# Kernel tuning notes

Measured on AMD Instinct MI355X. Metric: run time of the kernel, lower is better.

Reference implementation:

```python
import jax, jax.numpy as jnp
import numpy as np
from math import sqrt

D_MODEL = 1024
NUM_HEADS = 16
MASK_VAL = -100000000.0


def setup_inputs() -> dict:
    key = jax.random.key(0)
    k1, k2, k3, k4, k5 = jax.random.split(key, 5)
    scale = 1.0 / sqrt(D_MODEL)
    return {
        "in_features": jax.random.normal(k1, (2, 2048, D_MODEL), dtype=jnp.float32),
        "q_proj_weight": jax.random.normal(k2, (D_MODEL, D_MODEL), dtype=jnp.float32) * scale,
        "k_proj_weight": jax.random.normal(k3, (D_MODEL, D_MODEL), dtype=jnp.float32) * scale,
        "v_proj_weight": jax.random.normal(k4, (D_MODEL, D_MODEL), dtype=jnp.float32) * scale,
        "o_proj_weight": jax.random.normal(k5, (D_MODEL, D_MODEL), dtype=jnp.float32) * scale,
    }


def _proj_heads(x, w, h):
    # x: [b, s, d_in], w: [h*d, d_in] -> [b, h, s, d]
    d = w.shape[0] // h
    w = w.reshape(h, d, w.shape[1])
    return jnp.einsum('bsi,hdi->bhsd', x, w)


def reference(in_features, q_proj_weight, k_proj_weight, v_proj_weight, o_proj_weight):
    h = NUM_HEADS
    b, s, _ = in_features.shape
    q = _proj_heads(in_features, q_proj_weight, h)  # [b,h,s,dk]
    k = _proj_heads(in_features, k_proj_weight, h)
    v = _proj_heads(in_features, v_proj_weight, h)
    d_k = q.shape[-1]
    # additive causal mask: -1e8 above diagonal
    mask = jnp.triu(jnp.full((s, s), MASK_VAL, dtype=q.dtype), k=1)[None, None]
    scores = jnp.einsum('bhqd,bhkd->bhqk', q, k) / sqrt(d_k) + mask
    attn = jax.nn.softmax(scores, axis=-1)
    out = jnp.einsum('bhqk,bhkd->bhqd', attn, v)          # [b,h,s,dv]
    out = out.transpose(0, 2, 1, 3).reshape(b, s, -1)      # [b,s,h*dv]
    return jnp.einsum('bsv,mv->bsm', out, o_proj_weight)
```

## Files before the change

kernel.cpp:

```cpp
#include <hip/hip_runtime.h>
#include <hip/hip_bf16.h>
#include <stdint.h>
#include <type_traits>

typedef __bf16 bf16;
typedef __bf16 bf16x4 __attribute__((ext_vector_type(4)));
typedef __bf16 bf16x8 __attribute__((ext_vector_type(8)));
typedef float floatx4 __attribute__((ext_vector_type(4)));
typedef unsigned int u32;
typedef u32 u32x4 __attribute__((ext_vector_type(4)));

#define D_MODEL 1024
#define SEQ 2048
#define NHEADS 16
#define DH 64
#define BATCH 2
#define MROWS (BATCH * SEQ)

#define XELEMS ((size_t)MROWS * D_MODEL)
#define WELEMS ((size_t)D_MODEL * D_MODEL)
#define CVT_ELEMS (XELEMS + 4 * WELEMS)

__device__ __forceinline__ void gload_lds16(const void* g, void* l) {
  __builtin_amdgcn_global_load_lds(
      (const __attribute__((address_space(1))) u32*)g,
      (__attribute__((address_space(3))) u32*)l, 16, 0, 0);
}

__global__ __launch_bounds__(256) void cvt_f32_bf16(
    const float* __restrict__ s0, const float* __restrict__ s1,
    const float* __restrict__ s2, const float* __restrict__ s3,
    const float* __restrict__ s4, bf16* __restrict__ dst) {
  const size_t i = ((size_t)blockIdx.x * 256 + threadIdx.x) * 8;
  const float* src;
  size_t off;
  if (i < XELEMS) {
    src = s0; off = i;
  } else {
    const size_t j = i - XELEMS;
    const int r = (int)(j / WELEMS);
    src = (r == 0) ? s1 : (r == 1) ? s2 : (r == 2) ? s3 : s4;
    off = j - (size_t)r * WELEMS;
  }
  floatx4 f0 = *(const floatx4*)&src[off];
  floatx4 f1 = *(const floatx4*)&src[off + 4];
  bf16x8 o;
#pragma unroll
  for (int j = 0; j < 4; j++) { o[j] = (bf16)f0[j]; o[4 + j] = (bf16)f1[j]; }
  *(bf16x8*)&dst[i] = o;
}

#define QKV_ASLOT (256 * 64)
#define QKV_SLOT  (256 * 64 + 128 * 64)

__global__ __launch_bounds__(512) void gemm_qkv(
    const bf16* __restrict__ A, const bf16* __restrict__ W,
    bf16* __restrict__ Qo, bf16* __restrict__ Ko, bf16* __restrict__ Vto) {
  __shared__ bf16 sm[3 * QKV_SLOT];

  const int tid = threadIdx.x;
  const int lane = tid & 63;
  const int w = tid >> 6;
  const int lo16 = lane & 15;
  const int quad = lane >> 4;
  const int wy = w >> 1;
  const int wx = w & 1;

  const int n0 = blockIdx.x * 128;
  const int m0 = blockIdx.y * 256;

  const int sl = lane >> 3;
  const int sc = ((lane & 7) ^ sl) * 8;

  const floatx4 fz = {0.f, 0.f, 0.f, 0.f};
  floatx4 acc[4][4];
#pragma unroll
  for (int i = 0; i < 4; i++)
#pragma unroll
    for (int j = 0; j < 4; j++) acc[i][j] = fz;

  auto stage = [&](int t, int s) {
    bf16* As = &sm[s * QKV_SLOT];
    bf16* Bs = As + QKV_ASLOT;
    const int k0 = t * 64;
#pragma unroll
    for (int i = 0; i < 4; i++) {
      const int seg = w * 4 + i;
      const int row = seg * 8 + sl;
      gload_lds16(&A[(size_t)(m0 + row) * 1024 + k0 + sc], &As[seg * 512]);
    }
#pragma unroll
    for (int i = 0; i < 2; i++) {
      const int seg = w * 2 + i;
      const int row = seg * 8 + sl;
      gload_lds16(&W[(size_t)(n0 + row) * 1024 + k0 + sc], &Bs[seg * 512]);
    }
  };

  auto compute = [&](int s, auto vt) {
    constexpr bool VT = decltype(vt)::value;
    const bf16* As = &sm[s * QKV_SLOT];
    const bf16* Bs = As + QKV_ASLOT;
#pragma unroll
    for (int kk = 0; kk < 64; kk += 32) {
      bf16x8 af[4], bfr[4];
      const int cc = (kk >> 3) + quad;
#pragma unroll
      for (int t = 0; t < 4; t++) {
        const int ra = wy * 64 + t * 16 + lo16;
        const int rb = wx * 64 + t * 16 + lo16;
        af[t]  = *(const bf16x8*)&As[ra * 64 + ((cc ^ (ra & 7)) << 3)];
        bfr[t] = *(const bf16x8*)&Bs[rb * 64 + ((cc ^ (rb & 7)) << 3)];
      }
#pragma unroll
      for (int mt = 0; mt < 4; mt++)
#pragma unroll
        for (int nt = 0; nt < 4; nt++) {
          if constexpr (VT)
            acc[mt][nt] = __builtin_amdgcn_mfma_f32_16x16x32_bf16(bfr[nt], af[mt], acc[mt][nt], 0, 0, 0);
          else
            acc[mt][nt] = __builtin_amdgcn_mfma_f32_16x16x32_bf16(af[mt], bfr[nt], acc[mt][nt], 0, 0, 0);
        }
    }
  };

  auto step = [&](int t, int s, auto vt) {
    if (t + 2 < 16) stage(t + 2, (t + 2) % 3);
    compute(s, vt);
    if (t < 15) {
      if (t + 2 < 16) { asm volatile("s_waitcnt vmcnt(6)" ::: "memory"); }
      else            { asm volatile("s_waitcnt vmcnt(0)" ::: "memory"); }
      __builtin_amdgcn_s_barrier();
    }
  };

  auto mainloop = [&](auto vt) {
    stage(0, 0);
    stage(1, 1);
    asm volatile("s_waitcnt vmcnt(6)" ::: "memory");
    __builtin_amdgcn_s_barrier();
    for (int tb = 0; tb < 15; tb += 3) {
      step(tb + 0, 0, vt);
      step(tb + 1, 1, vt);
      step(tb + 2, 2, vt);
    }
    step(15, 0, vt);
  };
  if (n0 >= 2048) mainloop(std::true_type{}); else mainloop(std::false_type{});

  if (n0 < 2048) {
    bf16* C = (n0 < 1024) ? Qo : Ko;
    const int nc = (n0 < 1024) ? n0 : n0 - 1024;
#pragma unroll
    for (int mt = 0; mt < 4; mt++)
#pragma unroll
      for (int nt = 0; nt < 4; nt++)
#pragma unroll
        for (int r = 0; r < 4; r++) {
          const int row = m0 + wy * 64 + mt * 16 + quad * 4 + r;
          const int col = nc + wx * 64 + nt * 16 + lo16;
          C[(size_t)row * D_MODEL + col] = (bf16)acc[mt][nt][r];
        }
  } else {
    const int nv = n0 - 2048;
#pragma unroll
    for (int mt = 0; mt < 4; mt++)
#pragma unroll
      for (int nt = 0; nt < 4; nt++)
#pragma unroll
        for (int r = 0; r < 4; r++) {
          const int feat = nv + wx * 64 + nt * 16 + quad * 4 + r;
          const int tok  = m0 + wy * 64 + mt * 16 + lo16;
          const int hh = feat >> 6, dd = feat & 63;
          const int bb = tok >> 11, ss = tok & 2047;
          Vto[(size_t)((bb * NHEADS + hh) * DH + dd) * SEQ + ss] = (bf16)acc[mt][nt][r];
        }
  }
}

__global__ __launch_bounds__(256) void gemm_o(
    const bf16* __restrict__ A, const bf16* __restrict__ W,
    float* __restrict__ C) {
  __shared__ bf16 As[2 * 64 * 64];
  __shared__ bf16 Bs[2 * 128 * 64];

  const int tid = threadIdx.x;
  const int lane = tid & 63;
  const int w = tid >> 6;
  const int lo16 = lane & 15;
  const int quad = lane >> 4;
  const int wy = w >> 1, wx = w & 1;

  const int m0 = blockIdx.y * 64;
  const int n0 = blockIdx.x * 128;

  const int sl = lane >> 3;
  const int sc = ((lane & 7) ^ sl) * 8;

  const floatx4 fz = {0.f, 0.f, 0.f, 0.f};
  floatx4 acc[2][4];
#pragma unroll
  for (int i = 0; i < 2; i++)
#pragma unroll
    for (int j = 0; j < 4; j++) acc[i][j] = fz;

  for (int k0 = 0; k0 < 1024; k0 += 128) {
    __syncthreads();
#pragma unroll
    for (int kh = 0; kh < 2; kh++) {
#pragma unroll
      for (int i = 0; i < 2; i++) {
        const int seg = i * 4 + w;
        const int row = seg * 8 + sl;
        gload_lds16(&A[(size_t)(m0 + row) * 1024 + k0 + kh * 64 + sc],
                    &As[kh * 4096 + seg * 512]);
      }
#pragma unroll
      for (int i = 0; i < 4; i++) {
        const int seg = i * 4 + w;
        const int row = seg * 8 + sl;
        gload_lds16(&W[(size_t)(n0 + row) * 1024 + k0 + kh * 64 + sc],
                    &Bs[kh * 8192 + seg * 512]);
      }
    }
    __syncthreads();

#pragma unroll
    for (int kk = 0; kk < 128; kk += 32) {
      const int kh = kk >> 6;
      const int cc = ((kk & 63) >> 3) + quad;
      bf16x8 af[2], bfr[4];
#pragma unroll
      for (int t = 0; t < 2; t++) {
        const int ra = wy * 32 + t * 16 + lo16;
        af[t] = *(const bf16x8*)&As[kh * 4096 + ra * 64 + ((cc ^ (ra & 7)) << 3)];
      }
#pragma unroll
      for (int t = 0; t < 4; t++) {
        const int rb = wx * 64 + t * 16 + lo16;
        bfr[t] = *(const bf16x8*)&Bs[kh * 8192 + rb * 64 + ((cc ^ (rb & 7)) << 3)];
      }
#pragma unroll
      for (int mt = 0; mt < 2; mt++)
#pragma unroll
        for (int nt = 0; nt < 4; nt++)
          acc[mt][nt] = __builtin_amdgcn_mfma_f32_16x16x32_bf16(af[mt], bfr[nt], acc[mt][nt], 0, 0, 0);
    }
  }

#pragma unroll
  for (int mt = 0; mt < 2; mt++)
#pragma unroll
    for (int nt = 0; nt < 4; nt++)
#pragma unroll
      for (int r = 0; r < 4; r++) {
        const int row = m0 + wy * 32 + mt * 16 + quad * 4 + r;
        const int col = n0 + wx * 64 + nt * 16 + lo16;
        C[(size_t)row * D_MODEL + col] = acc[mt][nt][r];
      }
}

#define LPK 72
#define LPV 136

__global__ __launch_bounds__(512) void attn_causal(
    const bf16* __restrict__ Q, const bf16* __restrict__ Kg,
    const bf16* __restrict__ Vt, bf16* __restrict__ O) {
  __shared__ __align__(16) char smem[41984];
  bf16* Ks  = (bf16*)smem;
  bf16* VTs = (bf16*)(smem + 18432);
  float* Es = (float*)smem;

  const int tid = threadIdx.x;
  const int lane = tid & 63;
  const int wid = tid >> 6;
  const int g = wid >> 2;
  const int w4 = wid & 3;
  const int lo16 = lane & 15;
  const int quad = lane >> 4;

  const int x = blockIdx.x;
  const int qtA = x;
  const int qtB = 31 - x;
  const int nA = (qtA + 2) >> 1;
  const int nB = (qtB + 2) >> 1;
  const int h = blockIdx.y;
  const int b = blockIdx.z;
  const size_t base  = (size_t)b * SEQ * D_MODEL + (size_t)h * DH;
  const size_t baset = (size_t)(b * NHEADS + h) * DH * SEQ;

  const int rA = qtA * 64 + w4 * 16 + lo16;
  const int rB = qtB * 64 + w4 * 16 + lo16;
  bf16x8 qfA[2], qfB[2];
#pragma unroll
  for (int ks = 0; ks < 2; ks++) {
    qfA[ks] = *(const bf16x8*)&Q[base + (size_t)rA * D_MODEL + ks * 32 + quad * 8];
    qfB[ks] = *(const bf16x8*)&Q[base + (size_t)rB * D_MODEL + ks * 32 + quad * 8];
  }

  bf16x8 onesf;
#pragma unroll
  for (int j = 0; j < 8; j++) onesf[j] = (bf16)1.0f;

  const floatx4 fz = {0.f, 0.f, 0.f, 0.f};
  floatx4 oA[4], oB[4];
  floatx4 lA = fz, lB = fz;
#pragma unroll
  for (int i = 0; i < 4; i++) { oA[i] = fz; oB[i] = fz; }

  const int kr = tid >> 3;
  const int kc = (tid & 7) * 8;

  bf16x8 kvp[2], vvp[2];
#pragma unroll
  for (int c2 = 0; c2 < 2; c2++) {
    kvp[c2] = *(const bf16x8*)&Kg[base + (size_t)(c2 * 64 + kr) * D_MODEL + kc];
    vvp[c2] = *(const bf16x8*)&Vt[baset + (size_t)kr * SEQ + c2 * 64 + kc];
  }

  for (int c = 0; c < nB; c++) {
    const int j0 = c * 128;
    __syncthreads();
#pragma unroll
    for (int c2 = 0; c2 < 2; c2++) {
      *(bf16x8*)&Ks[(c2 * 64 + kr) * LPK + kc] = kvp[c2];
      *(bf16x8*)&VTs[kr * LPV + c2 * 64 + kc] = vvp[c2];
    }
    __syncthreads();

    if (c + 1 < nB) {
      const int j1 = j0 + 128;
#pragma unroll
      for (int c2 = 0; c2 < 2; c2++) {
        kvp[c2] = *(const bf16x8*)&Kg[base + (size_t)(j1 + c2 * 64 + kr) * D_MODEL + kc];
        vvp[c2] = *(const bf16x8*)&Vt[baset + (size_t)kr * SEQ + j1 + c2 * 64 + kc];
      }
    }

    auto compute = [&](int q0s, const bf16x8* qf, floatx4* oacc, floatx4& lacc,
                       bool diag) {
      floatx4 sacc[4];
#pragma unroll
      for (int n4 = 0; n4 < 4; n4++) sacc[n4] = fz;
#pragma unroll
      for (int n4 = 0; n4 < 4; n4++) {
        const int rk = g * 64 + n4 * 16 + lo16;
#pragma unroll
        for (int ks = 0; ks < 2; ks++) {
          bf16x8 kf = *(const bf16x8*)&Ks[rk * LPK + ks * 32 + quad * 8];
          sacc[n4] = __builtin_amdgcn_mfma_f32_16x16x32_bf16(kf, qf[ks], sacc[n4], 0, 0, 0);
        }
      }

      u32 wv[4][2];
      if (diag) {
        const int myq = q0s + w4 * 16 + lo16;
#pragma unroll
        for (int n4 = 0; n4 < 4; n4++) {
          float e[4];
#pragma unroll
          for (int r = 0; r < 4; r++) {
            const int kvb = j0 + g * 64 + n4 * 16 + quad * 4 + r;
            const float ev = __builtin_amdgcn_exp2f(fmaf(sacc[n4][r], 0.18033688f, -17.3123405f));
            e[r] = (kvb > myq) ? 0.f : ev;
          }
          asm("v_cvt_pk_bf16_f32 %0, %1, %2" : "=v"(wv[n4][0]) : "v"(e[0]), "v"(e[1]));
          asm("v_cvt_pk_bf16_f32 %0, %1, %2" : "=v"(wv[n4][1]) : "v"(e[2]), "v"(e[3]));
        }
      } else {
#pragma unroll
        for (int n4 = 0; n4 < 4; n4++) {
          float e[4];
#pragma unroll
          for (int r = 0; r < 4; r++)
            e[r] = __builtin_amdgcn_exp2f(fmaf(sacc[n4][r], 0.18033688f, -17.3123405f));
          asm("v_cvt_pk_bf16_f32 %0, %1, %2" : "=v"(wv[n4][0]) : "v"(e[0]), "v"(e[1]));
          asm("v_cvt_pk_bf16_f32 %0, %1, %2" : "=v"(wv[n4][1]) : "v"(e[2]), "v"(e[3]));
        }
      }

#pragma unroll
      for (int ks = 0; ks < 2; ks++) {
        u32 a0 = wv[2 * ks][0], b0 = wv[2 * ks + 1][0];
        u32 a1 = wv[2 * ks][1], b1 = wv[2 * ks + 1][1];
        asm("v_permlane32_swap_b32 %0, %1" : "+v"(a0), "+v"(b0));
        asm("v_permlane16_swap_b32 %0, %1" : "+v"(a0), "+v"(b0));
        asm("v_permlane32_swap_b32 %0, %1" : "+v"(a1), "+v"(b1));
        asm("v_permlane16_swap_b32 %0, %1" : "+v"(a1), "+v"(b1));
        u32x4 fw = {a0, a1, b0, b1};
        const bf16x8 pf = __builtin_bit_cast(bf16x8, fw);
#pragma unroll
        for (int dt = 0; dt < 4; dt++) {
          bf16x8 vf = *(const bf16x8*)&VTs[(dt * 16 + lo16) * LPV + g * 64 + ks * 32 + quad * 8];
          oacc[dt] = __builtin_amdgcn_mfma_f32_16x16x32_bf16(pf, vf, oacc[dt], 0, 0, 0);
        }
        lacc = __builtin_amdgcn_mfma_f32_16x16x32_bf16(pf, onesf, lacc, 0, 0, 0);
      }
    };

    compute(qtB * 64, qfB, oB, lB, c == nB - 1);
    if (c < nA) compute(qtA * 64, qfA, oA, lA, c == nA - 1);
  }

  __syncthreads();
  if (g == 1) {
    float* e = &Es[(w4 * 64 + lane) * 41];
#pragma unroll
    for (int dt = 0; dt < 4; dt++)
#pragma unroll
      for (int r = 0; r < 4; r++) e[dt * 4 + r] = oA[dt][r];
#pragma unroll
    for (int r = 0; r < 4; r++) e[16 + r] = lA[r];
#pragma unroll
    for (int dt = 0; dt < 4; dt++)
#pragma unroll
      for (int r = 0; r < 4; r++) e[20 + dt * 4 + r] = oB[dt][r];
#pragma unroll
    for (int r = 0; r < 4; r++) e[36 + r] = lB[r];
  }
  __syncthreads();
  if (g == 0) {
    const float* e = &Es[(w4 * 64 + lane) * 41];
#pragma unroll
    for (int dt = 0; dt < 4; dt++)
#pragma unroll
      for (int r = 0; r < 4; r++) { oA[dt][r] += e[dt * 4 + r]; oB[dt][r] += e[20 + dt * 4 + r]; }
#pragma unroll
    for (int r = 0; r < 4; r++) { lA[r] += e[16 + r]; lB[r] += e[36 + r]; }

    auto finish = [&](int q0s, floatx4* oacc, floatx4 lacc) {
#pragma unroll
      for (int r = 0; r < 4; r++) {
        const float inv = 1.0f / lacc[r];
        const int row = q0s + w4 * 16 + quad * 4 + r;
#pragma unroll
        for (int dt = 0; dt < 4; dt++)
          O[base + (size_t)row * D_MODEL + dt * 16 + lo16] = (bf16)(oacc[dt][r] * inv);
      }
    };
    finish(qtA * 64, oA, lA);
    finish(qtB * 64, oB, lB);
  }
}

extern "C" void kernel_launch(void* const* d_in, const int* in_sizes, int n_in,
                              void* d_out, int out_size, void* d_ws, size_t ws_size,
                              hipStream_t stream) {
  const float* X  = (const float*)d_in[0];
  const float* Wq = (const float*)d_in[1];
  const float* Wk = (const float*)d_in[2];
  const float* Wv = (const float*)d_in[3];
  const float* Wo = (const float*)d_in[4];
  float* out = (float*)d_out;

  bf16* cvt = (bf16*)d_ws;
  bf16* Xb  = cvt;
  bf16* Wqb = cvt + XELEMS;
  bf16* Wob = Wqb + 3 * WELEMS;
  bf16* Qb  = cvt + CVT_ELEMS;
  bf16* Kb  = Qb + XELEMS;
  bf16* Vtb = Kb + XELEMS;
  bf16* Ob  = Vtb + XELEMS;

  dim3 blk(256);
  cvt_f32_bf16<<<dim3((u32)(CVT_ELEMS / (256 * 8))), blk, 0, stream>>>(
      X, Wq, Wk, Wv, Wo, cvt);
  gemm_qkv<<<dim3(24, 16), dim3(512), 0, stream>>>(Xb, Wqb, Qb, Kb, Vtb);
  attn_causal<<<dim3(16, NHEADS, BATCH), dim3(512), 0, stream>>>(Qb, Kb, Vtb, Ob);
  gemm_o<<<dim3(8, 64), blk, 0, stream>>>(Ob, Wob, out);
}
```

Before: 170.2 us.

## Halve QKV GEMM tile height and interleave paired q-tile attention MFMAs

The QKV projection GEMM moves from 256x128 tiles to 128x128 tiles, with a 2x4 wave layout and a grid doubled to 768 blocks, so the GPU's compute units get more blocks and shared memory per block drops. The load wait counts are adjusted to match the smaller number of loads per stage. In the attention kernel, the two query tiles handled per block now share each K/V fragment load, and their QK and PV MFMAs are interleaved instead of computed one after the other, to expose more independent matrix work. The cost is more register pressure from holding two sets of score and probability fragments, and more reloading of the weight tiles in the GEMM.

```diff
diff --git a/kernel.cpp b/kernel.cpp
--- a/kernel.cpp
+++ b/kernel.cpp
@@ -50,8 +50,8 @@
   *(bf16x8*)&dst[i] = o;
 }
 
-#define QKV_ASLOT (256 * 64)
-#define QKV_SLOT  (256 * 64 + 128 * 64)
+#define QKV_ASLOT (128 * 64)
+#define QKV_SLOT  (2 * 128 * 64)
 
 __global__ __launch_bounds__(512) void gemm_qkv(
     const bf16* __restrict__ A, const bf16* __restrict__ W,
@@ -63,36 +63,31 @@
   const int w = tid >> 6;
   const int lo16 = lane & 15;
   const int quad = lane >> 4;
-  const int wy = w >> 1;
-  const int wx = w & 1;
+  const int wy = w >> 2;
+  const int wx = w & 3;
 
   const int n0 = blockIdx.x * 128;
-  const int m0 = blockIdx.y * 256;
+  const int m0 = blockIdx.y * 128;
 
   const int sl = lane >> 3;
   const int sc = ((lane & 7) ^ sl) * 8;
 
   const floatx4 fz = {0.f, 0.f, 0.f, 0.f};
-  floatx4 acc[4][4];
+  floatx4 acc[4][2];
 #pragma unroll
   for (int i = 0; i < 4; i++)
 #pragma unroll
-    for (int j = 0; j < 4; j++) acc[i][j] = fz;
+    for (int j = 0; j < 2; j++) acc[i][j] = fz;
 
   auto stage = [&](int t, int s) {
     bf16* As = &sm[s * QKV_SLOT];
     bf16* Bs = As + QKV_ASLOT;
     const int k0 = t * 64;
 #pragma unroll
-    for (int i = 0; i < 4; i++) {
-      const int seg = w * 4 + i;
-      const int row = seg * 8 + sl;
-      gload_lds16(&A[(size_t)(m0 + row) * 1024 + k0 + sc], &As[seg * 512]);
-    }
-#pragma unroll
     for (int i = 0; i < 2; i++) {
       const int seg = w * 2 + i;
       const int row = seg * 8 + sl;
+      gload_lds16(&A[(size_t)(m0 + row) * 1024 + k0 + sc], &As[seg * 512]);
       gload_lds16(&W[(size_t)(n0 + row) * 1024 + k0 + sc], &Bs[seg * 512]);
     }
   };
@@ -103,19 +98,22 @@
     const bf16* Bs = As + QKV_ASLOT;
 #pragma unroll
     for (int kk = 0; kk < 64; kk += 32) {
-      bf16x8 af[4], bfr[4];
+      bf16x8 af[4], bfr[2];
       const int cc = (kk >> 3) + quad;
 #pragma unroll
       for (int t = 0; t < 4; t++) {
         const int ra = wy * 64 + t * 16 + lo16;
-        const int rb = wx * 64 + t * 16 + lo16;
-        af[t]  = *(const bf16x8*)&As[ra * 64 + ((cc ^ (ra & 7)) << 3)];
+        af[t] = *(const bf16x8*)&As[ra * 64 + ((cc ^ (ra & 7)) << 3)];
+      }
+#pragma unroll
+      for (int t = 0; t < 2; t++) {
+        const int rb = wx * 32 + t * 16 + lo16;
         bfr[t] = *(const bf16x8*)&Bs[rb * 64 + ((cc ^ (rb & 7)) << 3)];
       }
 #pragma unroll
       for (int mt = 0; mt < 4; mt++)
 #pragma unroll
-        for (int nt = 0; nt < 4; nt++) {
+        for (int nt = 0; nt < 2; nt++) {
           if constexpr (VT)
             acc[mt][nt] = __builtin_amdgcn_mfma_f32_16x16x32_bf16(bfr[nt], af[mt], acc[mt][nt], 0, 0, 0);
           else
@@ -128,7 +126,7 @@
     if (t + 2 < 16) stage(t + 2, (t + 2) % 3);
     compute(s, vt);
     if (t < 15) {
-      if (t + 2 < 16) { asm volatile("s_waitcnt vmcnt(6)" ::: "memory"); }
+      if (t + 2 < 16) { asm volatile("s_waitcnt vmcnt(4)" ::: "memory"); }
       else            { asm volatile("s_waitcnt vmcnt(0)" ::: "memory"); }
       __builtin_amdgcn_s_barrier();
     }
@@ -137,7 +135,7 @@
   auto mainloop = [&](auto vt) {
     stage(0, 0);
     stage(1, 1);
-    asm volatile("s_waitcnt vmcnt(6)" ::: "memory");
+    asm volatile("s_waitcnt vmcnt(4)" ::: "memory");
     __builtin_amdgcn_s_barrier();
     for (int tb = 0; tb < 15; tb += 3) {
       step(tb + 0, 0, vt);
@@ -154,11 +152,11 @@
 #pragma unroll
     for (int mt = 0; mt < 4; mt++)
 #pragma unroll
-      for (int nt = 0; nt < 4; nt++)
+      for (int nt = 0; nt < 2; nt++)
 #pragma unroll
         for (int r = 0; r < 4; r++) {
           const int row = m0 + wy * 64 + mt * 16 + quad * 4 + r;
-          const int col = nc + wx * 64 + nt * 16 + lo16;
+          const int col = nc + wx * 32 + nt * 16 + lo16;
           C[(size_t)row * D_MODEL + col] = (bf16)acc[mt][nt][r];
         }
   } else {
@@ -166,10 +164,10 @@
 #pragma unroll
     for (int mt = 0; mt < 4; mt++)
 #pragma unroll
-      for (int nt = 0; nt < 4; nt++)
+      for (int nt = 0; nt < 2; nt++)
 #pragma unroll
         for (int r = 0; r < 4; r++) {
-          const int feat = nv + wx * 64 + nt * 16 + quad * 4 + r;
+          const int feat = nv + wx * 32 + nt * 16 + quad * 4 + r;
           const int tok  = m0 + wy * 64 + mt * 16 + lo16;
           const int hh = feat >> 6, dd = feat & 63;
           const int bb = tok >> 11, ss = tok & 2047;
@@ -337,22 +335,23 @@
       }
     }
 
-    auto compute = [&](int q0s, const bf16x8* qf, floatx4* oacc, floatx4& lacc,
-                       bool diag) {
-      floatx4 sacc[4];
-#pragma unroll
-      for (int n4 = 0; n4 < 4; n4++) sacc[n4] = fz;
-#pragma unroll
-      for (int n4 = 0; n4 < 4; n4++) {
-        const int rk = g * 64 + n4 * 16 + lo16;
-#pragma unroll
-        for (int ks = 0; ks < 2; ks++) {
-          bf16x8 kf = *(const bf16x8*)&Ks[rk * LPK + ks * 32 + quad * 8];
-          sacc[n4] = __builtin_amdgcn_mfma_f32_16x16x32_bf16(kf, qf[ks], sacc[n4], 0, 0, 0);
-        }
-      }
-
-      u32 wv[4][2];
+    const bool doA = (c < nA);
+
+    floatx4 sA[4], sB[4];
+#pragma unroll
+    for (int n4 = 0; n4 < 4; n4++) { sA[n4] = fz; sB[n4] = fz; }
+#pragma unroll
+    for (int n4 = 0; n4 < 4; n4++) {
+      const int rk = g * 64 + n4 * 16 + lo16;
+#pragma unroll
+      for (int ks = 0; ks < 2; ks++) {
+        bf16x8 kf = *(const bf16x8*)&Ks[rk * LPK + ks * 32 + quad * 8];
+        sB[n4] = __builtin_amdgcn_mfma_f32_16x16x32_bf16(kf, qfB[ks], sB[n4], 0, 0, 0);
+        if (doA) sA[n4] = __builtin_amdgcn_mfma_f32_16x16x32_bf16(kf, qfA[ks], sA[n4], 0, 0, 0);
+      }
+    }
+
+    auto pack = [&](const floatx4* sacc, int q0s, bool diag, u32 wv[4][2]) {
       if (diag) {
         const int myq = q0s + w4 * 16 + lo16;
 #pragma unroll
@@ -378,7 +377,9 @@
           asm("v_cvt_pk_bf16_f32 %0, %1, %2" : "=v"(wv[n4][1]) : "v"(e[2]), "v"(e[3]));
         }
       }
-
+    };
+
+    auto xpose = [&](u32 wv[4][2], u32x4 pf[2]) {
 #pragma unroll
       for (int ks = 0; ks < 2; ks++) {
         u32 a0 = wv[2 * ks][0], b0 = wv[2 * ks + 1][0];
@@ -388,18 +389,32 @@
         asm("v_permlane32_swap_b32 %0, %1" : "+v"(a1), "+v"(b1));
         asm("v_permlane16_swap_b32 %0, %1" : "+v"(a1), "+v"(b1));
         u32x4 fw = {a0, a1, b0, b1};
-        const bf16x8 pf = __builtin_bit_cast(bf16x8, fw);
-#pragma unroll
-        for (int dt = 0; dt < 4; dt++) {
-          bf16x8 vf = *(const bf16x8*)&VTs[(dt * 16 + lo16) * LPV + g * 64 + ks * 32 + quad * 8];
-          oacc[dt] = __builtin_amdgcn_mfma_f32_16x16x32_bf16(pf, vf, oacc[dt], 0, 0, 0);
-        }
-        lacc = __builtin_amdgcn_mfma_f32_16x16x32_bf16(pf, onesf, lacc, 0, 0, 0);
+        pf[ks] = fw;
       }
     };
 
-    compute(qtB * 64, qfB, oB, lB, c == nB - 1);
-    if (c < nA) compute(qtA * 64, qfA, oA, lA, c == nA - 1);
+    u32 wvB[4][2], wvA[4][2];
+    u32x4 pfB[2], pfA[2];
+    pack(sB, qtB * 64, c == nB - 1, wvB);
+    xpose(wvB, pfB);
+    if (doA) {
+      pack(sA, qtA * 64, c == nA - 1, wvA);
+      xpose(wvA, pfA);
+    }
+
+#pragma unroll
+    for (int ks = 0; ks < 2; ks++) {
+      const bf16x8 pb = __builtin_bit_cast(bf16x8, pfB[ks]);
+      const bf16x8 pa = __builtin_bit_cast(bf16x8, pfA[ks]);
+#pragma unroll
+      for (int dt = 0; dt < 4; dt++) {
+        bf16x8 vf = *(const bf16x8*)&VTs[(dt * 16 + lo16) * LPV + g * 64 + ks * 32 + quad * 8];
+        oB[dt] = __builtin_amdgcn_mfma_f32_16x16x32_bf16(pb, vf, oB[dt], 0, 0, 0);
+        if (doA) oA[dt] = __builtin_amdgcn_mfma_f32_16x16x32_bf16(pa, vf, oA[dt], 0, 0, 0);
+      }
+      lB = __builtin_amdgcn_mfma_f32_16x16x32_bf16(pb, onesf, lB, 0, 0, 0);
+      if (doA) lA = __builtin_amdgcn_mfma_f32_16x16x32_bf16(pa, onesf, lA, 0, 0, 0);
+    }
   }
 
   __syncthreads();
@@ -465,7 +480,7 @@
   dim3 blk(256);
   cvt_f32_bf16<<<dim3((u32)(CVT_ELEMS / (256 * 8))), blk, 0, stream>>>(
       X, Wq, Wk, Wv, Wo, cvt);
-  gemm_qkv<<<dim3(24, 16), dim3(512), 0, stream>>>(Xb, Wqb, Qb, Kb, Vtb);
+  gemm_qkv<<<dim3(24, 32), dim3(512), 0, stream>>>(Xb, Wqb, Qb, Kb, Vtb);
   attn_causal<<<dim3(16, NHEADS, BATCH), dim3(512), 0, stream>>>(Qb, Kb, Vtb, Ob);
   gemm_o<<<dim3(8, 64), blk, 0, stream>>>(Ob, Wob, out);
 }
```

After: 176.6 us. +3.7%, slower.

## Triple-buffer output projection GEMM with async LDS loads and vmcnt waits

Applied to the files above, without the earlier changes.

Restructures the o-projection GEMM from a two-barrier load-then-compute loop over 128-wide k chunks into a 3-slot ring of 64-wide k tiles. Global-to-LDS loads for tile t+2 are issued before computing tile t, with partial s_waitcnt vmcnt and a single barrier per step. This is meant to hide global memory latency behind the MFMA work. In exchange, shared memory per block grows to three slots, which may reduce occupancy.

```diff
diff --git a/kernel.cpp b/kernel.cpp
--- a/kernel.cpp
+++ b/kernel.cpp
@@ -178,11 +178,13 @@
   }
 }
 
+#define O_ASLOT (64 * 64)
+#define O_SLOT  (64 * 64 + 128 * 64)
+
 __global__ __launch_bounds__(256) void gemm_o(
     const bf16* __restrict__ A, const bf16* __restrict__ W,
     float* __restrict__ C) {
-  __shared__ bf16 As[2 * 64 * 64];
-  __shared__ bf16 Bs[2 * 128 * 64];
+  __shared__ bf16 sm[3 * O_SLOT];
 
   const int tid = threadIdx.x;
   const int lane = tid & 63;
@@ -204,41 +206,40 @@
 #pragma unroll
     for (int j = 0; j < 4; j++) acc[i][j] = fz;
 
-  for (int k0 = 0; k0 < 1024; k0 += 128) {
-    __syncthreads();
-#pragma unroll
-    for (int kh = 0; kh < 2; kh++) {
-#pragma unroll
-      for (int i = 0; i < 2; i++) {
-        const int seg = i * 4 + w;
-        const int row = seg * 8 + sl;
-        gload_lds16(&A[(size_t)(m0 + row) * 1024 + k0 + kh * 64 + sc],
-                    &As[kh * 4096 + seg * 512]);
-      }
-#pragma unroll
-      for (int i = 0; i < 4; i++) {
-        const int seg = i * 4 + w;
-        const int row = seg * 8 + sl;
-        gload_lds16(&W[(size_t)(n0 + row) * 1024 + k0 + kh * 64 + sc],
-                    &Bs[kh * 8192 + seg * 512]);
-      }
-    }
-    __syncthreads();
-
-#pragma unroll
-    for (int kk = 0; kk < 128; kk += 32) {
-      const int kh = kk >> 6;
-      const int cc = ((kk & 63) >> 3) + quad;
+  auto stage = [&](int t, int s) {
+    bf16* As = &sm[s * O_SLOT];
+    bf16* Bs = As + O_ASLOT;
+    const int k0 = t * 64;
+#pragma unroll
+    for (int i = 0; i < 2; i++) {
+      const int seg = w * 2 + i;
+      const int row = seg * 8 + sl;
+      gload_lds16(&A[(size_t)(m0 + row) * 1024 + k0 + sc], &As[seg * 512]);
+    }
+#pragma unroll
+    for (int i = 0; i < 4; i++) {
+      const int seg = w * 4 + i;
+      const int row = seg * 8 + sl;
+      gload_lds16(&W[(size_t)(n0 + row) * 1024 + k0 + sc], &Bs[seg * 512]);
+    }
+  };
+
+  auto compute = [&](int s) {
+    const bf16* As = &sm[s * O_SLOT];
+    const bf16* Bs = As + O_ASLOT;
+#pragma unroll
+    for (int kk = 0; kk < 64; kk += 32) {
+      const int cc = (kk >> 3) + quad;
       bf16x8 af[2], bfr[4];
 #pragma unroll
       for (int t = 0; t < 2; t++) {
         const int ra = wy * 32 + t * 16 + lo16;
-        af[t] = *(const bf16x8*)&As[kh * 4096 + ra * 64 + ((cc ^ (ra & 7)) << 3)];
+        af[t] = *(const bf16x8*)&As[ra * 64 + ((cc ^ (ra & 7)) << 3)];
       }
 #pragma unroll
       for (int t = 0; t < 4; t++) {
         const int rb = wx * 64 + t * 16 + lo16;
-        bfr[t] = *(const bf16x8*)&Bs[kh * 8192 + rb * 64 + ((cc ^ (rb & 7)) << 3)];
+        bfr[t] = *(const bf16x8*)&Bs[rb * 64 + ((cc ^ (rb & 7)) << 3)];
       }
 #pragma unroll
       for (int mt = 0; mt < 2; mt++)
@@ -246,7 +247,28 @@
         for (int nt = 0; nt < 4; nt++)
           acc[mt][nt] = __builtin_amdgcn_mfma_f32_16x16x32_bf16(af[mt], bfr[nt], acc[mt][nt], 0, 0, 0);
     }
-  }
+  };
+
+  auto step = [&](int t, int s) {
+    if (t + 2 < 16) stage(t + 2, (t + 2) % 3);
+    compute(s);
+    if (t < 15) {
+      if (t + 2 < 16) { asm volatile("s_waitcnt vmcnt(6)" ::: "memory"); }
+      else            { asm volatile("s_waitcnt vmcnt(0)" ::: "memory"); }
+      __builtin_amdgcn_s_barrier();
+    }
+  };
+
+  stage(0, 0);
+  stage(1, 1);
+  asm volatile("s_waitcnt vmcnt(6)" ::: "memory");
+  __builtin_amdgcn_s_barrier();
+  for (int tb = 0; tb < 15; tb += 3) {
+    step(tb + 0, 0);
+    step(tb + 1, 1);
+    step(tb + 2, 2);
+  }
+  step(15, 0);
 
 #pragma unroll
   for (int mt = 0; mt < 2; mt++)
```

Result: no change. 168.7 us (-0.8%).
